# Performance work log

Hardware: AMD Instinct MI355X
Metric: run time of the kernel (lower is better)

Reference implementation:

```python
import jax, jax.numpy as jnp
import numpy as np
import math

E = 1024      # hidden_dim = embed_dim (num_heads=1 so head_dim=E)
ND = 512      # output_dim = asymmetric value dim
N_DOMAIN = 2048
LN_EPS = 1e-5
SCALE = math.sqrt(1.0 / E) * 2.0 * math.log(N_DOMAIN)


def layernorm(x, g, b):
    mu = jnp.mean(x, axis=-1, keepdims=True)
    var = jnp.var(x, axis=-1, keepdims=True)
    return (x - mu) * jax.lax.rsqrt(var + LN_EPS) * g + b


def setup_inputs() -> dict:
    key = jax.random.key(0)
    ks = jax.random.split(key, 5)
    B, L = 8, 2048
    return {
        "x": jax.random.normal(ks[0], (B, L, E), dtype=jnp.float32),
        "in_proj_w": jax.random.normal(ks[1], (2 * E + ND, E), dtype=jnp.float32) * 0.02,
        "w1": jax.random.normal(ks[2], (2048, ND), dtype=jnp.float32) * 0.02,
        "b1": jnp.zeros((2048,), dtype=jnp.float32),
        "w2": jax.random.normal(ks[3], (ND, 2048), dtype=jnp.float32) * 0.02,
        "b2": jnp.zeros((ND,), dtype=jnp.float32),
        "g1": jnp.ones((ND,), dtype=jnp.float32),
        "be1": jnp.zeros((ND,), dtype=jnp.float32),
        "g2": jnp.ones((ND,), dtype=jnp.float32),
        "be2": jnp.zeros((ND,), dtype=jnp.float32),
    }


def reference(x, in_proj_w, w1, b1, w2, b2, g1, be1, g2, be2):
    # fused in-projection (no bias): q,k get E dims, v gets ND dims
    proj = jnp.einsum("ble,fe->blf", x, in_proj_w)
    q = proj[..., :E]
    k = proj[..., E:2 * E]
    v = proj[..., 2 * E:]
    # custom scale: sqrt(1/head_dim) * 2 * log(N)
    scores = jnp.einsum("bld,bsd->bls", q * SCALE, k)  # [B, L, S]
    attn_w = jax.nn.softmax(scores, axis=-1)
    attn_out = jnp.einsum("bls,bsd->bld", attn_w, v)   # [B, L, ND] (no out proj)
    # skip=False (hidden_dim != output_dim): norm1(attn) only
    h = layernorm(attn_out, g1, be1)
    ff = jnp.einsum("bld,fd->blf", h, w1) + b1
    ff = jnp.einsum("blf,df->bld", jax.nn.relu(ff), w2) + b2
    return layernorm(h + ff, g2, be2)
```

## Files before the change

### kernel.cpp

```cpp
#include <hip/hip_runtime.h>
#include <hip/hip_bf16.h>

typedef unsigned short u16;
typedef unsigned int u32;
typedef float f32x4 __attribute__((ext_vector_type(4)));
typedef _Float16 f16x8 __attribute__((ext_vector_type(8)));
typedef u32 u32x4 __attribute__((ext_vector_type(4)));
typedef u32 u32x2 __attribute__((ext_vector_type(2)));

#define SEQ 2048
#define EDIM 1024

__device__ __forceinline__ u16 f2h(float f) {
  _Float16 h = (_Float16)f;
  return __builtin_bit_cast(u16, h);
}
__device__ __forceinline__ float h2f(u16 u) {
  return (float)__builtin_bit_cast(_Float16, u);
}
__device__ __forceinline__ u32 pk(float a, float b) {
  return (u32)f2h(a) | ((u32)f2h(b) << 16);
}

#define N_X  2097152
#define N_WP 327680
#define N_W1 131072
#define N_W2 131072
__global__ __launch_bounds__(256) void cvt_all(const float* __restrict__ x, u16* __restrict__ xb,
                                               const float* __restrict__ wp, u16* __restrict__ wpb,
                                               const float* __restrict__ w1, u16* __restrict__ w1b,
                                               const float* __restrict__ w2, u16* __restrict__ w2b) {
  int i = blockIdx.x * 256 + threadIdx.x;
  const float* src; u16* dst; int li;
  if (i < N_X) { src = x; dst = xb; li = i; }
  else if (i < N_X + N_WP) { src = wp; dst = wpb; li = i - N_X; }
  else if (i < N_X + N_WP + N_W1) { src = w1; dst = w1b; li = i - N_X - N_WP; }
  else if (i < N_X + N_WP + N_W1 + N_W2) { src = w2; dst = w2b; li = i - N_X - N_WP - N_W1; }
  else return;
  const f32x4* p = (const f32x4*)(src + (size_t)li * 8);
  f32x4 a = p[0], b = p[1];
  u32x4 o = {pk(a[0], a[1]), pk(a[2], a[3]), pk(b[0], b[1]), pk(b[2], b[3])};
  *(u32x4*)(dst + (size_t)li * 8) = o;
}

struct GemmP {
  const u16* A; const u16* B;
  int lda, ldb, K;
  long bsA, bsB, bsC;
  int ldc;
  u16* Cb;
  const float* bias;
  const u16* resid;
  u16* qk; u16* vT;
  float scale;
};

template <int EPI>
__global__ __launch_bounds__(512, 2) void gemm256(GemmP p) {
  __shared__ __align__(16) char lds[131072];
  const int tid = threadIdx.x;
  const int lane = tid & 63;
  const int wave = tid >> 6;
  const int wm = wave >> 2, wn = wave & 3;
  const int bn0 = blockIdx.x * 256;
  const int bm0 = blockIdx.y * 256;
  const int z = blockIdx.z;

  const u16* gA[4]; const u16* gB[4];
  int ldsA[4], ldsB[4];
  {
    const u16* Ab = p.A + (long)z * p.bsA + (long)bm0 * p.lda;
    const u16* Bb = p.B + (long)z * p.bsB + (long)bn0 * p.ldb;
#pragma unroll
    for (int i = 0; i < 4; ++i) {
      int ch = i * 512 + tid;
      int row = ch >> 3, s = ch & 7;
      int ks = ((s ^ (row & 7)) << 3);
      gA[i] = Ab + (long)row * p.lda + ks;
      gB[i] = Bb + (long)row * p.ldb + ks;
      ldsA[i] = ch * 16;
      ldsB[i] = 32768 + ch * 16;
    }
  }
  auto stage = [&](int buf) {
    char* dst = lds + buf * 65536;
#pragma unroll
    for (int i = 0; i < 4; ++i) {
      __builtin_amdgcn_global_load_lds(
          (const __attribute__((address_space(1))) u32*)gA[i],
          (__attribute__((address_space(3))) u32*)(dst + ldsA[i]), 16, 0, 0);
      gA[i] += 64;
    }
#pragma unroll
    for (int i = 0; i < 4; ++i) {
      __builtin_amdgcn_global_load_lds(
          (const __attribute__((address_space(1))) u32*)gB[i],
          (__attribute__((address_space(3))) u32*)(dst + ldsB[i]), 16, 0, 0);
      gB[i] += 64;
    }
  };

  int abase[2], bbase[2];
  {
    int rA = wm * 128 + (lane & 15);
    int sA = (lane >> 4) ^ (lane & 7);
    abase[0] = rA * 128 + (sA << 4);
    abase[1] = abase[0] ^ 64;
    int rB = wn * 64 + (lane & 15);
    int sB = (lane >> 4) ^ (lane & 7);
    bbase[0] = 32768 + rB * 128 + (sB << 4);
    bbase[1] = bbase[0] ^ 64;
  }

  f32x4 acc[8][4] = {};
  stage(0);
  const int nk = p.K >> 6;
  int cur = 0;
  for (int kt = 0; kt < nk; ++kt) {
    __syncthreads();
    if (kt + 1 < nk) stage(cur ^ 1);
    const char* base = lds + cur * 65536;
#pragma unroll
    for (int h = 0; h < 2; ++h) {
      f16x8 av[8], bv[4];
#pragma unroll
      for (int m = 0; m < 8; ++m) av[m] = *(const f16x8*)(base + abase[h] + m * 2048);
#pragma unroll
      for (int j = 0; j < 4; ++j) bv[j] = *(const f16x8*)(base + bbase[h] + j * 2048);
#pragma unroll
      for (int m = 0; m < 8; ++m)
#pragma unroll
        for (int j = 0; j < 4; ++j)
          acc[m][j] = __builtin_amdgcn_mfma_f32_16x16x32_f16(av[m], bv[j], acc[m][j], 0, 0, 0);
    }
    cur ^= 1;
  }

#pragma unroll
  for (int i = 0; i < 8; ++i) {
#pragma unroll
    for (int j = 0; j < 4; ++j) {
      int mb = bm0 + wm * 128 + i * 16 + ((lane >> 4) << 2);
      int n = bn0 + wn * 64 + j * 16 + (lane & 15);
      if constexpr (EPI == 1) {
        int b = mb >> 11, l0 = mb & 2047;
        if (n < EDIM) {
          u16* dst = p.qk + (long)b * 4194304 + (long)l0 * 1024 + n;
#pragma unroll
          for (int r = 0; r < 4; ++r) dst[r * 1024] = f2h(acc[i][j][r] * p.scale);
        } else if (n < 2 * EDIM) {
          u16* dst = p.qk + (long)b * 4194304 + 2097152 + (long)l0 * 1024 + (n - EDIM);
#pragma unroll
          for (int r = 0; r < 4; ++r) dst[r * 1024] = f2h(acc[i][j][r]);
        } else {
          u16* dst = p.vT + (long)b * 1048576 + (long)(n - 2 * EDIM) * 2048 + l0;
          u32x2 w = {pk(acc[i][j][0], acc[i][j][1]), pk(acc[i][j][2], acc[i][j][3])};
          *(u32x2*)dst = w;
        }
      } else if constexpr (EPI == 2) {
        u16* dst = p.Cb + (long)mb * p.ldc + n;
        float bias = p.bias[n];
#pragma unroll
        for (int r = 0; r < 4; ++r) dst[(long)r * p.ldc] = f2h(fmaxf(acc[i][j][r] + bias, 0.f));
      } else {
        u16* dst = p.Cb + (long)z * p.bsC + (long)mb * p.ldc + n;
#pragma unroll
        for (int r = 0; r < 4; ++r) dst[(long)r * p.ldc] = f2h(acc[i][j][r]);
      }
    }
  }
}

template <int EPI>
__global__ __launch_bounds__(256) void gemm_bt(GemmP p) {
  __shared__ __align__(16) char lds[65536];
  const int tid = threadIdx.x;
  const int lane = tid & 63;
  const int wave = tid >> 6;
  const int wm = wave >> 1, wn = wave & 1;
  const int bn0 = blockIdx.x * 128;
  const int bm0 = blockIdx.y * 128;
  const int z = blockIdx.z;

  const u16* gA[4]; const u16* gB[4];
  int ldsA[4], ldsB[4];
  {
    const u16* Ab = p.A + (long)z * p.bsA + (long)bm0 * p.lda;
    const u16* Bb = p.B + (long)z * p.bsB + (long)bn0 * p.ldb;
#pragma unroll
    for (int i = 0; i < 4; ++i) {
      int ch = i * 256 + tid;
      int row = ch >> 3, s = ch & 7;
      int ks = ((s ^ (row & 7)) << 3);
      gA[i] = Ab + (long)row * p.lda + ks;
      gB[i] = Bb + (long)row * p.ldb + ks;
      ldsA[i] = ch * 16;
      ldsB[i] = 16384 + ch * 16;
    }
  }
  auto stage = [&](int buf) {
    char* dst = lds + buf * 32768;
#pragma unroll
    for (int i = 0; i < 4; ++i) {
      __builtin_amdgcn_global_load_lds(
          (const __attribute__((address_space(1))) u32*)gA[i],
          (__attribute__((address_space(3))) u32*)(dst + ldsA[i]), 16, 0, 0);
      gA[i] += 64;
    }
#pragma unroll
    for (int i = 0; i < 4; ++i) {
      __builtin_amdgcn_global_load_lds(
          (const __attribute__((address_space(1))) u32*)gB[i],
          (__attribute__((address_space(3))) u32*)(dst + ldsB[i]), 16, 0, 0);
      gB[i] += 64;
    }
  };

  int ao[2][4], bo[2][4];
#pragma unroll
  for (int h = 0; h < 2; ++h) {
#pragma unroll
    for (int i = 0; i < 4; ++i) {
      int rA = wm * 64 + i * 16 + (lane & 15);
      ao[h][i] = rA * 128 + ((((h << 2) | (lane >> 4)) ^ (rA & 7)) << 4);
      int rB = wn * 64 + i * 16 + (lane & 15);
      bo[h][i] = 16384 + rB * 128 + ((((h << 2) | (lane >> 4)) ^ (rB & 7)) << 4);
    }
  }

  f32x4 acc[4][4] = {};
  stage(0);
  const int nk = p.K >> 6;
  int cur = 0;
  for (int kt = 0; kt < nk; ++kt) {
    __syncthreads();
    if (kt + 1 < nk) stage(cur ^ 1);
    const char* base = lds + cur * 32768;
#pragma unroll
    for (int h = 0; h < 2; ++h) {
      f16x8 av[4], bv[4];
#pragma unroll
      for (int i = 0; i < 4; ++i) av[i] = *(const f16x8*)(base + ao[h][i]);
#pragma unroll
      for (int j = 0; j < 4; ++j) bv[j] = *(const f16x8*)(base + bo[h][j]);
#pragma unroll
      for (int i = 0; i < 4; ++i)
#pragma unroll
        for (int j = 0; j < 4; ++j)
          acc[i][j] = __builtin_amdgcn_mfma_f32_16x16x32_f16(av[i], bv[j], acc[i][j], 0, 0, 0);
    }
    cur ^= 1;
  }

#pragma unroll
  for (int i = 0; i < 4; ++i) {
#pragma unroll
    for (int j = 0; j < 4; ++j) {
      int mb = bm0 + wm * 64 + i * 16 + ((lane >> 4) << 2);
      int n = bn0 + wn * 64 + j * 16 + (lane & 15);
      if constexpr (EPI == 3) {
        float bias = p.bias[n];
        u16* dst = p.Cb + (long)mb * 512 + n;
        const u16* rs = p.resid + (long)mb * 512 + n;
#pragma unroll
        for (int r = 0; r < 4; ++r) dst[r * 512] = f2h(acc[i][j][r] + bias + h2f(rs[r * 512]));
      } else {
        u16* dst = p.Cb + (long)z * p.bsC + (long)mb * p.ldc + n;
#pragma unroll
        for (int r = 0; r < 4; ++r) dst[(long)r * p.ldc] = f2h(acc[i][j][r]);
      }
    }
  }
}

__global__ __launch_bounds__(256) void softmax_rows(const u16* __restrict__ S,
                                                    u16* __restrict__ W, int b0) {
  int r = blockIdx.x;
  int z = r >> 11, l = r & 2047;
  int tid = threadIdx.x, lane = tid & 63, wv = tid >> 6;
  const u16* x = S + (long)r * 2048 + tid * 8;
  u32x4 raw = *(const u32x4*)x;
  float e[8];
#pragma unroll
  for (int q = 0; q < 4; ++q) {
    e[2 * q] = h2f((u16)(raw[q] & 0xffff));
    e[2 * q + 1] = h2f((u16)(raw[q] >> 16));
  }
  float m = e[0];
#pragma unroll
  for (int q = 1; q < 8; ++q) m = fmaxf(m, e[q]);
#pragma unroll
  for (int off = 32; off; off >>= 1) m = fmaxf(m, __shfl_xor(m, off));
  __shared__ float red[8];
  if (lane == 0) red[wv] = m;
  __syncthreads();
  m = fmaxf(fmaxf(red[0], red[1]), fmaxf(red[2], red[3]));
  float s = 0.f;
#pragma unroll
  for (int q = 0; q < 8; ++q) { e[q] = __expf(e[q] - m); s += e[q]; }
#pragma unroll
  for (int off = 32; off; off >>= 1) s += __shfl_xor(s, off);
  if (lane == 0) red[4 + wv] = s;
  __syncthreads();
  s = red[4] + red[5] + red[6] + red[7];
  float inv = 1.f / s;
  u32x4 o = {pk(e[0] * inv, e[1] * inv), pk(e[2] * inv, e[3] * inv),
             pk(e[4] * inv, e[5] * inv), pk(e[6] * inv, e[7] * inv)};
  *(u32x4*)(W + (long)(b0 + z) * 4194304 + (long)l * 2048 + tid * 8) = o;
}

template <int INF16, int OUTF16>
__global__ __launch_bounds__(256) void ln_rows(const void* __restrict__ X,
                                               const float* __restrict__ g,
                                               const float* __restrict__ bb,
                                               void* __restrict__ out) {
  int row = blockIdx.x * 4 + (threadIdx.x >> 6);
  int lane = threadIdx.x & 63;
  float v[8];
  if constexpr (INF16) {
    u32x4 raw = *(const u32x4*)((const u16*)X + (long)row * 512 + lane * 8);
#pragma unroll
    for (int q = 0; q < 4; ++q) {
      v[2 * q] = h2f((u16)(raw[q] & 0xffff));
      v[2 * q + 1] = h2f((u16)(raw[q] >> 16));
    }
  } else {
    const float* x = (const float*)X + (long)row * 512 + lane * 8;
    f32x4 a = *(const f32x4*)x, b = *(const f32x4*)(x + 4);
#pragma unroll
    for (int q = 0; q < 4; ++q) { v[q] = a[q]; v[4 + q] = b[q]; }
  }
  float s = 0.f, sq = 0.f;
#pragma unroll
  for (int q = 0; q < 8; ++q) { s += v[q]; sq += v[q] * v[q]; }
#pragma unroll
  for (int off = 32; off; off >>= 1) {
    s += __shfl_xor(s, off);
    sq += __shfl_xor(sq, off);
  }
  float mean = s * (1.f / 512.f);
  float var = sq * (1.f / 512.f) - mean * mean;
  float rstd = rsqrtf(var + 1e-5f);
  f32x4 g0 = *(const f32x4*)(g + lane * 8), g1v = *(const f32x4*)(g + lane * 8 + 4);
  f32x4 b0 = *(const f32x4*)(bb + lane * 8), b1v = *(const f32x4*)(bb + lane * 8 + 4);
  float o[8];
#pragma unroll
  for (int q = 0; q < 4; ++q) o[q] = (v[q] - mean) * rstd * g0[q] + b0[q];
#pragma unroll
  for (int q = 0; q < 4; ++q) o[4 + q] = (v[4 + q] - mean) * rstd * g1v[q] + b1v[q];
  if constexpr (OUTF16) {
    u32x4 pkd = {pk(o[0], o[1]), pk(o[2], o[3]), pk(o[4], o[5]), pk(o[6], o[7])};
    *(u32x4*)((u16*)out + (long)row * 512 + lane * 8) = pkd;
  } else {
    float* dst = (float*)out + (long)row * 512 + lane * 8;
    *(f32x4*)dst = (f32x4){o[0], o[1], o[2], o[3]};
    *(f32x4*)(dst + 4) = (f32x4){o[4], o[5], o[6], o[7]};
  }
}

extern "C" void kernel_launch(void* const* d_in, const int* in_sizes, int n_in,
                              void* d_out, int out_size, void* d_ws, size_t ws_size,
                              hipStream_t stream) {
  const float* x = (const float*)d_in[0];
  const float* wp = (const float*)d_in[1];
  const float* w1 = (const float*)d_in[2];
  const float* b1 = (const float*)d_in[3];
  const float* w2 = (const float*)d_in[4];
  const float* b2 = (const float*)d_in[5];
  const float* g1 = (const float*)d_in[6];
  const float* be1 = (const float*)d_in[7];
  const float* g2 = (const float*)d_in[8];
  const float* be2 = (const float*)d_in[9];

  char* ws = (char*)d_ws;
  size_t off = 0;
  auto alloc = [&](size_t bytes) {
    char* p = ws + off;
    off += (bytes + 255) & ~(size_t)255;
    return p;
  };
  u16* wpb = (u16*)alloc(2560 * 1024 * 2);
  u16* w1b = (u16*)alloc(2048 * 512 * 2);
  u16* w2b = (u16*)alloc(512 * 2048 * 2);
  char* xb_region = alloc(33554432);
  u16* qk = (u16*)alloc(67108864);
  u16* vT = (u16*)alloc(16777216);
  u16* hb = (u16*)alloc(16777216);
  int bpl = (ws_size >= off + (size_t)67108864) ? 8 : 4;
  char* sc_region = alloc((size_t)bpl * 2048 * 2048 * 2);
  if (off > ws_size) return;

  u16* xb = (u16*)xb_region;
  u16* attn16 = (u16*)xb_region;
  u16* scores = (u16*)sc_region;
  u16* y16 = (u16*)sc_region;
  u16* ff1 = qk;

  const float SC = (float)(0.03125 * 2.0 * 7.6246189861593985);

  cvt_all<<<dim3(10496), dim3(256), 0, stream>>>(x, xb, wp, wpb, w1, w1b, w2, w2b);

  {
    GemmP p{};
    p.A = xb; p.lda = 1024; p.B = wpb; p.ldb = 1024; p.K = 1024;
    p.qk = qk; p.vT = vT; p.scale = SC;
    gemm256<1><<<dim3(10, 64, 1), 512, 0, stream>>>(p);
  }

  for (int it = 0; it < 8 / bpl; ++it) {
    int b0 = it * bpl;
    GemmP p{};
    p.A = qk + (long)b0 * 4194304; p.lda = 1024; p.bsA = 4194304;
    p.B = qk + (long)b0 * 4194304 + 2097152; p.ldb = 1024; p.bsB = 4194304;
    p.K = 1024; p.Cb = scores; p.ldc = 2048; p.bsC = 4194304;
    gemm256<4><<<dim3(8, 8, bpl), 512, 0, stream>>>(p);
    softmax_rows<<<dim3(bpl * 2048), dim3(256), 0, stream>>>(scores, qk, b0);
  }

  {
    GemmP p{};
    p.A = qk; p.lda = 2048; p.bsA = 4194304;
    p.B = vT; p.ldb = 2048; p.bsB = 1048576;
    p.K = 2048; p.Cb = attn16; p.ldc = 512; p.bsC = 1048576;
    gemm_bt<4><<<dim3(4, 16, 8), 256, 0, stream>>>(p);
  }

  ln_rows<1, 1><<<dim3(4096), dim3(256), 0, stream>>>(attn16, g1, be1, hb);

  {
    GemmP p{};
    p.A = hb; p.lda = 512; p.B = w1b; p.ldb = 512; p.K = 512;
    p.Cb = ff1; p.ldc = 2048; p.bias = b1;
    gemm256<2><<<dim3(8, 64, 1), 512, 0, stream>>>(p);
  }

  {
    GemmP p{};
    p.A = ff1; p.lda = 2048; p.B = w2b; p.ldb = 2048; p.K = 2048;
    p.Cb = y16; p.bias = b2; p.resid = hb;
    gemm_bt<3><<<dim3(4, 128, 1), 256, 0, stream>>>(p);
  }

  ln_rows<1, 0><<<dim3(4096), dim3(256), 0, stream>>>(y16, g2, be2, (float*)d_out);
}
```

Measured before the change: 376.5 us.

## Use 128-tile GEMM for in-projection and one-wave-per-row softmax

The QKV in-projection moves from the 256x256-tile gemm256 kernel to the 128x128-tile gemm_bt kernel, which gets the EPI==1 scatter epilogue. The goal is more blocks (2560 instead of 640) to spread the 16384x2560 GEMM more evenly across CUs. Softmax now gives each 2048-wide row to a single wave that handles 32 elements per lane, dropping the LDS reductions and __syncthreads. The trade-off is lower per-block reuse in the GEMM and more registers per softmax thread.

```diff
diff --git a/kernel.cpp b/kernel.cpp
--- a/kernel.cpp
+++ b/kernel.cpp
@@ -56,6 +56,123 @@
 };
 
 template <int EPI>
+__global__ __launch_bounds__(256) void gemm_bt(GemmP p) {
+  __shared__ __align__(16) char lds[65536];
+  const int tid = threadIdx.x;
+  const int lane = tid & 63;
+  const int wave = tid >> 6;
+  const int wm = wave >> 1, wn = wave & 1;
+  const int bn0 = blockIdx.x * 128;
+  const int bm0 = blockIdx.y * 128;
+  const int z = blockIdx.z;
+
+  const u16* gA[4]; const u16* gB[4];
+  int ldsA[4], ldsB[4];
+  {
+    const u16* Ab = p.A + (long)z * p.bsA + (long)bm0 * p.lda;
+    const u16* Bb = p.B + (long)z * p.bsB + (long)bn0 * p.ldb;
+#pragma unroll
+    for (int i = 0; i < 4; ++i) {
+      int ch = i * 256 + tid;
+      int row = ch >> 3, s = ch & 7;
+      int ks = ((s ^ (row & 7)) << 3);
+      gA[i] = Ab + (long)row * p.lda + ks;
+      gB[i] = Bb + (long)row * p.ldb + ks;
+      ldsA[i] = ch * 16;
+      ldsB[i] = 16384 + ch * 16;
+    }
+  }
+  auto stage = [&](int buf) {
+    char* dst = lds + buf * 32768;
+#pragma unroll
+    for (int i = 0; i < 4; ++i) {
+      __builtin_amdgcn_global_load_lds(
+          (const __attribute__((address_space(1))) u32*)gA[i],
+          (__attribute__((address_space(3))) u32*)(dst + ldsA[i]), 16, 0, 0);
+      gA[i] += 64;
+    }
+#pragma unroll
+    for (int i = 0; i < 4; ++i) {
+      __builtin_amdgcn_global_load_lds(
+          (const __attribute__((address_space(1))) u32*)gB[i],
+          (__attribute__((address_space(3))) u32*)(dst + ldsB[i]), 16, 0, 0);
+      gB[i] += 64;
+    }
+  };
+
+  int ao[2][4], bo[2][4];
+#pragma unroll
+  for (int h = 0; h < 2; ++h) {
+#pragma unroll
+    for (int i = 0; i < 4; ++i) {
+      int rA = wm * 64 + i * 16 + (lane & 15);
+      ao[h][i] = rA * 128 + ((((h << 2) | (lane >> 4)) ^ (rA & 7)) << 4);
+      int rB = wn * 64 + i * 16 + (lane & 15);
+      bo[h][i] = 16384 + rB * 128 + ((((h << 2) | (lane >> 4)) ^ (rB & 7)) << 4);
+    }
+  }
+
+  f32x4 acc[4][4] = {};
+  stage(0);
+  const int nk = p.K >> 6;
+  int cur = 0;
+  for (int kt = 0; kt < nk; ++kt) {
+    __syncthreads();
+    if (kt + 1 < nk) stage(cur ^ 1);
+    const char* base = lds + cur * 32768;
+#pragma unroll
+    for (int h = 0; h < 2; ++h) {
+      f16x8 av[4], bv[4];
+#pragma unroll
+      for (int i = 0; i < 4; ++i) av[i] = *(const f16x8*)(base + ao[h][i]);
+#pragma unroll
+      for (int j = 0; j < 4; ++j) bv[j] = *(const f16x8*)(base + bo[h][j]);
+#pragma unroll
+      for (int i = 0; i < 4; ++i)
+#pragma unroll
+        for (int j = 0; j < 4; ++j)
+          acc[i][j] = __builtin_amdgcn_mfma_f32_16x16x32_f16(av[i], bv[j], acc[i][j], 0, 0, 0);
+    }
+    cur ^= 1;
+  }
+
+#pragma unroll
+  for (int i = 0; i < 4; ++i) {
+#pragma unroll
+    for (int j = 0; j < 4; ++j) {
+      int mb = bm0 + wm * 64 + i * 16 + ((lane >> 4) << 2);
+      int n = bn0 + wn * 64 + j * 16 + (lane & 15);
+      if constexpr (EPI == 1) {
+        int b = mb >> 11, l0 = mb & 2047;
+        if (n < EDIM) {
+          u16* dst = p.qk + (long)b * 4194304 + (long)l0 * 1024 + n;
+#pragma unroll
+          for (int r = 0; r < 4; ++r) dst[r * 1024] = f2h(acc[i][j][r] * p.scale);
+        } else if (n < 2 * EDIM) {
+          u16* dst = p.qk + (long)b * 4194304 + 2097152 + (long)l0 * 1024 + (n - EDIM);
+#pragma unroll
+          for (int r = 0; r < 4; ++r) dst[r * 1024] = f2h(acc[i][j][r]);
+        } else {
+          u16* dst = p.vT + (long)b * 1048576 + (long)(n - 2 * EDIM) * 2048 + l0;
+          u32x2 w = {pk(acc[i][j][0], acc[i][j][1]), pk(acc[i][j][2], acc[i][j][3])};
+          *(u32x2*)dst = w;
+        }
+      } else if constexpr (EPI == 3) {
+        float bias = p.bias[n];
+        u16* dst = p.Cb + (long)mb * 512 + n;
+        const u16* rs = p.resid + (long)mb * 512 + n;
+#pragma unroll
+        for (int r = 0; r < 4; ++r) dst[r * 512] = f2h(acc[i][j][r] + bias + h2f(rs[r * 512]));
+      } else {
+        u16* dst = p.Cb + (long)z * p.bsC + (long)mb * p.ldc + n;
+#pragma unroll
+        for (int r = 0; r < 4; ++r) dst[(long)r * p.ldc] = f2h(acc[i][j][r]);
+      }
+    }
+  }
+}
+
+template <int EPI>
 __global__ __launch_bounds__(512, 2) void gemm256(GemmP p) {
   __shared__ __align__(16) char lds[131072];
   const int tid = threadIdx.x;
@@ -142,22 +259,7 @@
     for (int j = 0; j < 4; ++j) {
       int mb = bm0 + wm * 128 + i * 16 + ((lane >> 4) << 2);
       int n = bn0 + wn * 64 + j * 16 + (lane & 15);
-      if constexpr (EPI == 1) {
-        int b = mb >> 11, l0 = mb & 2047;
-        if (n < EDIM) {
-          u16* dst = p.qk + (long)b * 4194304 + (long)l0 * 1024 + n;
-#pragma unroll
-          for (int r = 0; r < 4; ++r) dst[r * 1024] = f2h(acc[i][j][r] * p.scale);
-        } else if (n < 2 * EDIM) {
-          u16* dst = p.qk + (long)b * 4194304 + 2097152 + (long)l0 * 1024 + (n - EDIM);
-#pragma unroll
-          for (int r = 0; r < 4; ++r) dst[r * 1024] = f2h(acc[i][j][r]);
-        } else {
-          u16* dst = p.vT + (long)b * 1048576 + (long)(n - 2 * EDIM) * 2048 + l0;
-          u32x2 w = {pk(acc[i][j][0], acc[i][j][1]), pk(acc[i][j][2], acc[i][j][3])};
-          *(u32x2*)dst = w;
-        }
-      } else if constexpr (EPI == 2) {
+      if constexpr (EPI == 2) {
         u16* dst = p.Cb + (long)mb * p.ldc + n;
         float bias = p.bias[n];
 #pragma unroll
@@ -171,142 +273,43 @@
   }
 }
 
-template <int EPI>
-__global__ __launch_bounds__(256) void gemm_bt(GemmP p) {
-  __shared__ __align__(16) char lds[65536];
-  const int tid = threadIdx.x;
-  const int lane = tid & 63;
-  const int wave = tid >> 6;
-  const int wm = wave >> 1, wn = wave & 1;
-  const int bn0 = blockIdx.x * 128;
-  const int bm0 = blockIdx.y * 128;
-  const int z = blockIdx.z;
-
-  const u16* gA[4]; const u16* gB[4];
-  int ldsA[4], ldsB[4];
-  {
-    const u16* Ab = p.A + (long)z * p.bsA + (long)bm0 * p.lda;
-    const u16* Bb = p.B + (long)z * p.bsB + (long)bn0 * p.ldb;
-#pragma unroll
-    for (int i = 0; i < 4; ++i) {
-      int ch = i * 256 + tid;
-      int row = ch >> 3, s = ch & 7;
-      int ks = ((s ^ (row & 7)) << 3);
-      gA[i] = Ab + (long)row * p.lda + ks;
-      gB[i] = Bb + (long)row * p.ldb + ks;
-      ldsA[i] = ch * 16;
-      ldsB[i] = 16384 + ch * 16;
-    }
-  }
-  auto stage = [&](int buf) {
-    char* dst = lds + buf * 32768;
-#pragma unroll
-    for (int i = 0; i < 4; ++i) {
-      __builtin_amdgcn_global_load_lds(
-          (const __attribute__((address_space(1))) u32*)gA[i],
-          (__attribute__((address_space(3))) u32*)(dst + ldsA[i]), 16, 0, 0);
-      gA[i] += 64;
-    }
-#pragma unroll
-    for (int i = 0; i < 4; ++i) {
-      __builtin_amdgcn_global_load_lds(
-          (const __attribute__((address_space(1))) u32*)gB[i],
-          (__attribute__((address_space(3))) u32*)(dst + ldsB[i]), 16, 0, 0);
-      gB[i] += 64;
-    }
-  };
-
-  int ao[2][4], bo[2][4];
-#pragma unroll
-  for (int h = 0; h < 2; ++h) {
-#pragma unroll
-    for (int i = 0; i < 4; ++i) {
-      int rA = wm * 64 + i * 16 + (lane & 15);
-      ao[h][i] = rA * 128 + ((((h << 2) | (lane >> 4)) ^ (rA & 7)) << 4);
-      int rB = wn * 64 + i * 16 + (lane & 15);
-      bo[h][i] = 16384 + rB * 128 + ((((h << 2) | (lane >> 4)) ^ (rB & 7)) << 4);
-    }
-  }
-
-  f32x4 acc[4][4] = {};
-  stage(0);
-  const int nk = p.K >> 6;
-  int cur = 0;
-  for (int kt = 0; kt < nk; ++kt) {
-    __syncthreads();
-    if (kt + 1 < nk) stage(cur ^ 1);
-    const char* base = lds + cur * 32768;
-#pragma unroll
-    for (int h = 0; h < 2; ++h) {
-      f16x8 av[4], bv[4];
-#pragma unroll
-      for (int i = 0; i < 4; ++i) av[i] = *(const f16x8*)(base + ao[h][i]);
-#pragma unroll
-      for (int j = 0; j < 4; ++j) bv[j] = *(const f16x8*)(base + bo[h][j]);
-#pragma unroll
-      for (int i = 0; i < 4; ++i)
-#pragma unroll
-        for (int j = 0; j < 4; ++j)
-          acc[i][j] = __builtin_amdgcn_mfma_f32_16x16x32_f16(av[i], bv[j], acc[i][j], 0, 0, 0);
-    }
-    cur ^= 1;
-  }
-
-#pragma unroll
-  for (int i = 0; i < 4; ++i) {
-#pragma unroll
-    for (int j = 0; j < 4; ++j) {
-      int mb = bm0 + wm * 64 + i * 16 + ((lane >> 4) << 2);
-      int n = bn0 + wn * 64 + j * 16 + (lane & 15);
-      if constexpr (EPI == 3) {
-        float bias = p.bias[n];
-        u16* dst = p.Cb + (long)mb * 512 + n;
-        const u16* rs = p.resid + (long)mb * 512 + n;
-#pragma unroll
-        for (int r = 0; r < 4; ++r) dst[r * 512] = f2h(acc[i][j][r] + bias + h2f(rs[r * 512]));
-      } else {
-        u16* dst = p.Cb + (long)z * p.bsC + (long)mb * p.ldc + n;
-#pragma unroll
-        for (int r = 0; r < 4; ++r) dst[(long)r * p.ldc] = f2h(acc[i][j][r]);
-      }
-    }
-  }
-}
-
 __global__ __launch_bounds__(256) void softmax_rows(const u16* __restrict__ S,
                                                     u16* __restrict__ W, int b0) {
-  int r = blockIdx.x;
-  int z = r >> 11, l = r & 2047;
-  int tid = threadIdx.x, lane = tid & 63, wv = tid >> 6;
-  const u16* x = S + (long)r * 2048 + tid * 8;
-  u32x4 raw = *(const u32x4*)x;
-  float e[8];
-#pragma unroll
-  for (int q = 0; q < 4; ++q) {
-    e[2 * q] = h2f((u16)(raw[q] & 0xffff));
-    e[2 * q + 1] = h2f((u16)(raw[q] >> 16));
-  }
+  int row = blockIdx.x * 4 + (threadIdx.x >> 6);
+  int lane = threadIdx.x & 63;
+  int z = row >> 11, l = row & 2047;
+  const u16* x = S + (long)row * 2048 + lane * 32;
+  u32x4 raw[4];
+#pragma unroll
+  for (int c = 0; c < 4; ++c) raw[c] = ((const u32x4*)x)[c];
+  float e[32];
+#pragma unroll
+  for (int c = 0; c < 4; ++c)
+#pragma unroll
+    for (int q = 0; q < 4; ++q) {
+      e[c * 8 + 2 * q] = h2f((u16)(raw[c][q] & 0xffff));
+      e[c * 8 + 2 * q + 1] = h2f((u16)(raw[c][q] >> 16));
+    }
   float m = e[0];
 #pragma unroll
-  for (int q = 1; q < 8; ++q) m = fmaxf(m, e[q]);
+  for (int q = 1; q < 32; ++q) m = fmaxf(m, e[q]);
 #pragma unroll
   for (int off = 32; off; off >>= 1) m = fmaxf(m, __shfl_xor(m, off));
-  __shared__ float red[8];
-  if (lane == 0) red[wv] = m;
-  __syncthreads();
-  m = fmaxf(fmaxf(red[0], red[1]), fmaxf(red[2], red[3]));
   float s = 0.f;
 #pragma unroll
-  for (int q = 0; q < 8; ++q) { e[q] = __expf(e[q] - m); s += e[q]; }
+  for (int q = 0; q < 32; ++q) { e[q] = __expf(e[q] - m); s += e[q]; }
 #pragma unroll
   for (int off = 32; off; off >>= 1) s += __shfl_xor(s, off);
-  if (lane == 0) red[4 + wv] = s;
-  __syncthreads();
-  s = red[4] + red[5] + red[6] + red[7];
   float inv = 1.f / s;
-  u32x4 o = {pk(e[0] * inv, e[1] * inv), pk(e[2] * inv, e[3] * inv),
-             pk(e[4] * inv, e[5] * inv), pk(e[6] * inv, e[7] * inv)};
-  *(u32x4*)(W + (long)(b0 + z) * 4194304 + (long)l * 2048 + tid * 8) = o;
+  u16* dst = W + (long)(b0 + z) * 4194304 + (long)l * 2048 + lane * 32;
+#pragma unroll
+  for (int c = 0; c < 4; ++c) {
+    u32x4 o = {pk(e[c * 8 + 0] * inv, e[c * 8 + 1] * inv),
+               pk(e[c * 8 + 2] * inv, e[c * 8 + 3] * inv),
+               pk(e[c * 8 + 4] * inv, e[c * 8 + 5] * inv),
+               pk(e[c * 8 + 6] * inv, e[c * 8 + 7] * inv)};
+    ((u32x4*)dst)[c] = o;
+  }
 }
 
 template <int INF16, int OUTF16>
@@ -404,7 +407,7 @@
     GemmP p{};
     p.A = xb; p.lda = 1024; p.B = wpb; p.ldb = 1024; p.K = 1024;
     p.qk = qk; p.vT = vT; p.scale = SC;
-    gemm256<1><<<dim3(10, 64, 1), 512, 0, stream>>>(p);
+    gemm_bt<1><<<dim3(20, 128, 1), 256, 0, stream>>>(p);
   }
 
   for (int it = 0; it < 8 / bpl; ++it) {
@@ -414,7 +417,7 @@
     p.B = qk + (long)b0 * 4194304 + 2097152; p.ldb = 1024; p.bsB = 4194304;
     p.K = 1024; p.Cb = scores; p.ldc = 2048; p.bsC = 4194304;
     gemm256<4><<<dim3(8, 8, bpl), 512, 0, stream>>>(p);
-    softmax_rows<<<dim3(bpl * 2048), dim3(256), 0, stream>>>(scores, qk, b0);
+    softmax_rows<<<dim3(bpl * 512), dim3(256), 0, stream>>>(scores, qk, b0);
   }
 
   {
```

Result: slower. 386.3 us (+2.6%).
